# Performance work log

Measured on AMD Instinct MI355X. Metric: run time of the kernel, lower is better.

The kernel has to match this reference:

```python
import jax, jax.numpy as jnp
import numpy as np

NUM_HEADS = 16


def setup_inputs() -> dict:
    key = jax.random.key(0)
    k = jax.random.split(key, 5)
    b, s, h = 2, 2048, 1024
    scale = 1.0 / np.sqrt(h)
    return {
        "x": jax.random.normal(k[0], (b, s, h), dtype=jnp.float32),
        "W_qkv": jax.random.normal(k[1], (h, 3 * h), dtype=jnp.float32) * scale,
        "b_qkv": jax.random.normal(k[2], (3 * h,), dtype=jnp.float32) * 0.02,
        "W_o": jax.random.normal(k[3], (h, h), dtype=jnp.float32) * scale,
        "b_o": jax.random.normal(k[4], (h,), dtype=jnp.float32) * 0.02,
    }


def _mha_causal(Q, K, V, num_heads):
    b, s, hd = Q.shape
    d_head = hd // num_heads
    # b s (n h) -> b n s h
    _Q = Q.reshape(b, s, num_heads, d_head).transpose(0, 2, 1, 3)
    _K = K.reshape(b, s, num_heads, d_head).transpose(0, 2, 1, 3)
    _V = V.reshape(b, s, num_heads, d_head).transpose(0, 2, 1, 3)
    scores = jnp.einsum('bnqh,bnkh->bnqk', _Q, _K)
    causal = jnp.tril(jnp.ones((s, s), dtype=bool))  # True where allowed
    scores = jnp.where(causal, scores, -jnp.inf) / jnp.sqrt(jnp.float32(d_head))
    A = jax.nn.softmax(scores, axis=-1)
    AV = jnp.einsum('bnqk,bnkh->bnqh', A, _V)
    return AV.transpose(0, 2, 1, 3).reshape(b, s, hd)


def reference(x, W_qkv, b_qkv, W_o, b_o):
    qkv = x @ W_qkv + b_qkv  # [b, s, 3h]
    Q, K, V = jnp.split(qkv, 3, axis=-1)
    attn = _mha_causal(Q, K, V, NUM_HEADS)
    return attn @ W_o + b_o
```

## Files before the change

### kernel.cpp

```cpp
#include <hip/hip_runtime.h>
#include <hip/hip_bf16.h>

typedef unsigned short u16;
typedef __attribute__((ext_vector_type(8))) short short8;
typedef __attribute__((ext_vector_type(4))) float f32x4;
typedef __attribute__((ext_vector_type(16))) float f32x16;
typedef __attribute__((ext_vector_type(4))) float float4v;
typedef __attribute__((ext_vector_type(4))) unsigned int uint4v;
typedef __attribute__((ext_vector_type(2))) unsigned int uint2v;

__device__ __forceinline__ u16 f2bf(float f) {
    union { float f; unsigned u; } x;
    x.f = f;
    unsigned r = x.u + 0x7fffu + ((x.u >> 16) & 1u);
    return (u16)(r >> 16);
}

__device__ __forceinline__ unsigned cvtpk(float lo, float hi) {
    unsigned r;
    asm("v_cvt_pk_bf16_f32 %0, %1, %2" : "=v"(r) : "v"(lo), "v"(hi));
    return r;
}

__device__ __forceinline__ void gload16(const u16* g, u16* l) {
    __builtin_amdgcn_global_load_lds(
        (const __attribute__((address_space(1))) unsigned*)g,
        (__attribute__((address_space(3))) unsigned*)l, 16, 0, 0);
}

#define WAITV(n) asm volatile("s_waitcnt vmcnt(" #n ")" ::: "memory")

__global__ __launch_bounds__(256) void prep(
    const float* __restrict__ x, const float* __restrict__ Wqkv,
    const float* __restrict__ Wo, u16* __restrict__ x_bf,
    u16* __restrict__ wqkvT, u16* __restrict__ woT) {
    int bid = blockIdx.x;
    int t = threadIdx.x;
    if (bid < 2048) {
        int i = bid * 256 + t;
        const float4v* s = (const float4v*)(x + (size_t)i * 8);
        float4v a = s[0], b = s[1];
        uint4v o;
        o[0] = (unsigned)f2bf(a[0]) | ((unsigned)f2bf(a[1]) << 16);
        o[1] = (unsigned)f2bf(a[2]) | ((unsigned)f2bf(a[3]) << 16);
        o[2] = (unsigned)f2bf(b[0]) | ((unsigned)f2bf(b[1]) << 16);
        o[3] = (unsigned)f2bf(b[2]) | ((unsigned)f2bf(b[3]) << 16);
        *(uint4v*)(x_bf + (size_t)i * 8) = o;
        return;
    }
    const float* src;
    u16* dst;
    int C, tid;
    if (bid < 2816) { tid = bid - 2048; src = Wqkv; dst = wqkvT; C = 3072; }
    else            { tid = bid - 2816; src = Wo;   dst = woT;   C = 1024; }
    int tr = (tid & 15) * 64;
    int tc = (tid >> 4) * 64;
    __shared__ __align__(16) u16 tile[64][72];
    int r = t >> 2;
    int c4 = (t & 3) * 16;
    const float4v* sp = (const float4v*)(src + (size_t)(tr + r) * C + tc + c4);
#pragma unroll
    for (int v = 0; v < 4; v++) {
        float4v xv = sp[v];
#pragma unroll
        for (int j = 0; j < 4; j++) tile[r][c4 + v * 4 + j] = f2bf(xv[j]);
    }
    __syncthreads();
    u16* dp = dst + (size_t)(tc + r) * 1024 + tr + c4;
#pragma unroll
    for (int i = 0; i < 16; i++) dp[i] = tile[c4 + i][r];
}

__global__ __launch_bounds__(256) void gemm_qkv(
    const u16* __restrict__ A, const u16* __restrict__ BT,
    const float* __restrict__ bias, u16* __restrict__ qbuf,
    u16* __restrict__ kvp) {
    const int K = 1024;
    __shared__ __align__(16) u16 SMEM[24576];
    int bm = blockIdx.x, bn = blockIdx.y;
    int t = threadIdx.x;
    int lane = t & 63, wave = t >> 6;
    int wr = wave >> 1, wc = wave & 1;
    f32x4 acc[4][4] = {};

    const u16* gA = A + (size_t)(bm * 128) * K;
    const u16* gB = BT + (size_t)(bn * 128) * K;

    auto stage = [&](int buf, int k0) {
#pragma unroll
        for (int i = 0; i < 2; i++) {
            int o = i * 4096 + t * 16;
            int row = o >> 6;
            int cb = (o & 63) ^ (((row >> 1) & 3) << 4);
            gload16(gA + (size_t)row * K + k0 + (cb >> 1),
                    &SMEM[buf * 4096 + i * 2048 + (t & 192) * 8]);
        }
#pragma unroll
        for (int i = 0; i < 2; i++) {
            int o = i * 4096 + t * 16;
            int row = o >> 6;
            int cb = (o & 63) ^ (((row >> 1) & 3) << 4);
            gload16(gB + (size_t)row * K + k0 + (cb >> 1),
                    &SMEM[12288 + buf * 4096 + i * 2048 + (t & 192) * 8]);
        }
    };

    stage(0, 0);
    stage(1, 32);
    WAITV(4);
    __builtin_amdgcn_s_barrier();

    for (int tt = 0; tt < 32; tt++) {
        bool pre = (tt + 2 < 32);
        if (pre) stage((tt + 2) % 3, (tt + 2) << 5);
        int row16 = lane & 15;
        int colb = ((lane >> 4) * 16) ^ (((row16 >> 1) & 3) << 4);
        const u16* Ab = &SMEM[(tt % 3) * 4096];
        const u16* Bb = &SMEM[12288 + (tt % 3) * 4096];
        short8 af[4], bf[4];
#pragma unroll
        for (int m = 0; m < 4; m++)
            af[m] = *(const short8*)&Ab[(wr * 64 + m * 16 + row16) * 32 + (colb >> 1)];
#pragma unroll
        for (int n = 0; n < 4; n++)
            bf[n] = *(const short8*)&Bb[(wc * 64 + n * 16 + row16) * 32 + (colb >> 1)];
        __builtin_amdgcn_s_setprio(1);
#pragma unroll
        for (int m = 0; m < 4; m++)
#pragma unroll
            for (int n = 0; n < 4; n++)
                acc[m][n] = __builtin_amdgcn_mfma_f32_16x16x32_bf16(
                    af[m], bf[n], acc[m][n], 0, 0, 0);
        __builtin_amdgcn_s_setprio(0);
        if (pre) { WAITV(4); } else { WAITV(0); }
        __builtin_amdgcn_s_barrier();
    }

    int l15 = lane & 15, hi = lane >> 4;
    if (bn < 8) {
#pragma unroll
        for (int m = 0; m < 4; m++)
#pragma unroll
            for (int n = 0; n < 4; n++) {
                int col = bn * 128 + wc * 64 + n * 16 + l15;
                float bv = bias[col];
#pragma unroll
                for (int r = 0; r < 4; r++) {
                    int row = bm * 128 + wr * 64 + m * 16 + hi * 4 + r;
                    qbuf[(size_t)row * 1024 + col] = f2bf(acc[m][n][r] + bv);
                }
            }
    } else if (bn < 16) {
        int h2 = (bn - 8) * 2 + wc;
#pragma unroll
        for (int m = 0; m < 4; m++)
#pragma unroll
            for (int n = 0; n < 4; n++) {
                int d = n * 16 + l15;
                float bv = bias[1024 + h2 * 64 + d];
#pragma unroll
                for (int r = 0; r < 4; r++) {
                    int row = bm * 128 + wr * 64 + m * 16 + hi * 4 + r;
                    int b = row >> 11;
                    int tt = (row & 2047) >> 6;
                    int k = row & 63;
                    kvp[(size_t)(b * 16 + h2) * 262144 + tt * 8192 + k * 64 + d] =
                        f2bf(acc[m][n][r] + bv);
                }
            }
    } else {
        int h2 = (bn - 16) * 2 + wc;
        int rowbase = bm * 128 + wr * 64;
        int b = rowbase >> 11;
        int tt = (rowbase & 2047) >> 6;
        u16* wl = &SMEM[wave * 4608];
#pragma unroll
        for (int m = 0; m < 4; m++)
#pragma unroll
            for (int n = 0; n < 4; n++) {
                int d = n * 16 + l15;
                float bv = bias[2048 + h2 * 64 + d];
                unsigned p0 = cvtpk(acc[m][n][0] + bv, acc[m][n][1] + bv);
                unsigned p1 = cvtpk(acc[m][n][2] + bv, acc[m][n][3] + bv);
                *(uint2v*)&wl[d * 72 + m * 16 + hi * 4] = (uint2v){p0, p1};
            }
        u16* dst = kvp + (size_t)(b * 16 + h2) * 262144 + tt * 8192 + 4096;
#pragma unroll
        for (int i = 0; i < 8; i++)
            *(uint4v*)(dst + lane * 64 + i * 8) = *(const uint4v*)&wl[lane * 72 + i * 8];
    }
}

__global__ __launch_bounds__(256) void gemm_out(
    const u16* __restrict__ A, const u16* __restrict__ BT,
    const float* __restrict__ bias, float* __restrict__ Cout) {
    const int K = 1024, N = 1024;
    __shared__ __align__(16) u16 As[3][4096];
    __shared__ __align__(16) u16 Bs[3][2048];
    int bm = blockIdx.x, bn = blockIdx.y;
    int t = threadIdx.x;
    int lane = t & 63, wave = t >> 6;
    int wr = wave >> 1, wc = wave & 1;
    f32x4 acc[4][2] = {};

    const u16* gA = A + (size_t)(bm * 128) * K;
    const u16* gB = BT + (size_t)(bn * 64) * K;

    auto stage = [&](int buf, int k0) {
#pragma unroll
        for (int i = 0; i < 2; i++) {
            int o = i * 4096 + t * 16;
            int row = o >> 6;
            int cb = (o & 63) ^ (((row >> 1) & 3) << 4);
            gload16(gA + (size_t)row * K + k0 + (cb >> 1),
                    &As[buf][i * 2048 + (t & 192) * 8]);
        }
        {
            int o = t * 16;
            int row = o >> 6;
            int cb = (o & 63) ^ (((row >> 1) & 3) << 4);
            gload16(gB + (size_t)row * K + k0 + (cb >> 1),
                    &Bs[buf][(t & 192) * 8]);
        }
    };

    stage(0, 0);
    stage(1, 32);
    WAITV(3);
    __builtin_amdgcn_s_barrier();

    for (int tt = 0; tt < 32; tt++) {
        bool pre = (tt + 2 < 32);
        if (pre) stage((tt + 2) % 3, (tt + 2) << 5);
        int row16 = lane & 15;
        int colb = ((lane >> 4) * 16) ^ (((row16 >> 1) & 3) << 4);
        short8 af[4], bf[2];
#pragma unroll
        for (int m = 0; m < 4; m++)
            af[m] = *(const short8*)&As[tt % 3][(wr * 64 + m * 16 + row16) * 32 + (colb >> 1)];
#pragma unroll
        for (int n = 0; n < 2; n++)
            bf[n] = *(const short8*)&Bs[tt % 3][(wc * 32 + n * 16 + row16) * 32 + (colb >> 1)];
        __builtin_amdgcn_s_setprio(1);
#pragma unroll
        for (int m = 0; m < 4; m++)
#pragma unroll
            for (int n = 0; n < 2; n++)
                acc[m][n] = __builtin_amdgcn_mfma_f32_16x16x32_bf16(
                    bf[n], af[m], acc[m][n], 0, 0, 0);
        __builtin_amdgcn_s_setprio(0);
        if (pre) { WAITV(3); } else { WAITV(0); }
        __builtin_amdgcn_s_barrier();
    }

    int l15 = lane & 15, hi = lane >> 4;
#pragma unroll
    for (int m = 0; m < 4; m++)
#pragma unroll
        for (int n = 0; n < 2; n++) {
            int col0 = bn * 64 + wc * 32 + n * 16 + hi * 4;
            float4v bv = *(const float4v*)&bias[col0];
            int row = bm * 128 + wr * 64 + m * 16 + l15;
            float4v v = {acc[m][n][0] + bv[0], acc[m][n][1] + bv[1],
                         acc[m][n][2] + bv[2], acc[m][n][3] + bv[3]};
            *(float4v*)(Cout + (size_t)row * N + col0) = v;
        }
}

__global__ __launch_bounds__(256, 2) void attn_kernel(
    const u16* __restrict__ qbuf, const u16* __restrict__ kvp,
    u16* __restrict__ attn, float* __restrict__ part_o,
    float* __restrict__ part_l) {
    int bid = blockIdx.x;
    int bh = bid & 31;
    int j = 23 - (bid >> 5);
    int sp, tbeg, tend, kc = 0;
    bool partial;
    if (j >= 8) {
        int idx = j - 8;
        sp = 8 + (idx >> 1);
        kc = idx & 1;
        int half = sp + 1;
        partial = true;
        tbeg = kc ? half : 0;
        tend = kc ? 2 * sp + 2 : half;
    } else {
        sp = j;
        partial = false;
        tbeg = 0;
        tend = 2 * sp + 2;
    }
    int b = bh >> 4, h = bh & 15;
    int t = threadIdx.x;
    int lane = t & 63, w = t >> 6;
    int qb = sp * 128 + w * 32;
    int kend = qb + 32;
    int l31 = lane & 31, hi32 = lane >> 5;
    int swz = (lane & 7) << 4;

    __shared__ __align__(16) u16 KVb[24576];

    const u16* kvb = kvp + (size_t)bh * 262144;

    auto stage = [&](int buf, int tt) {
        const char* g0 = (const char*)(kvb + (size_t)tt * 8192);
#pragma unroll
        for (int kv2 = 0; kv2 < 2; kv2++)
#pragma unroll
            for (int i = 0; i < 2; i++) {
                int o = i * 4096 + t * 16;
                int row = o >> 7;
                int cb = (o & 127) ^ ((row & 7) << 4);
                gload16((const u16*)(g0 + kv2 * 8192 + row * 128 + cb),
                        &KVb[buf * 8192 + kv2 * 4096 + i * 2048 + (t & 192) * 8]);
            }
    };

    short8 qf[4];
    {
        const u16* q0 = qbuf + (size_t)(b * 2048 + qb + l31) * 1024 + h * 64 + hi32 * 8;
#pragma unroll
        for (int dd = 0; dd < 4; dd++) qf[dd] = *(const short8*)(q0 + dd * 16);
    }
    stage(tbeg % 3, tbeg);
    stage((tbeg + 1) % 3, tbeg + 1);

    float l_lane = 0.f;
    f32x16 oT[2] = {};

    const float C1 = 0.1803368880f;
    const float C2 = -17.3123404907f;

    WAITV(4);
    __builtin_amdgcn_s_barrier();

    for (int tt = tbeg; tt < tend; tt++) {
        bool pre = (tt + 2 < tend);
        if (pre) stage((tt + 2) % 3, tt + 2);
        int k0 = tt * 64;
        if (k0 < kend) {
            const u16* Ks = &KVb[(tt % 3) * 8192];
            const u16* Vs = Ks + 4096;
            f32x16 sc[2];
            __builtin_amdgcn_s_setprio(1);
#pragma unroll
            for (int kb = 0; kb < 2; kb++) {
                f32x16 z = {};
#pragma unroll
                for (int dd = 0; dd < 4; dd++) {
                    int off = (kb * 32 + l31) * 64 + (((dd * 32 + hi32 * 16) ^ swz) >> 1);
                    short8 kf = *(const short8*)&Ks[off];
                    z = __builtin_amdgcn_mfma_f32_32x32x16_bf16(kf, qf[dd], z, 0, 0, 0);
                }
                sc[kb] = z;
            }
            __builtin_amdgcn_s_setprio(0);

            float p[2][16];
            int q_g = qb + l31;
            if (k0 + 64 > qb) {
#pragma unroll
                for (int kb = 0; kb < 2; kb++)
#pragma unroll
                    for (int r = 0; r < 16; r++) {
                        int kg = k0 + kb * 32 + (r & 3) + 8 * (r >> 2) + 4 * hi32;
                        float v = (kg <= q_g) ? sc[kb][r] : -1e30f;
                        float pe = __builtin_amdgcn_exp2f(fmaf(v, C1, C2));
                        p[kb][r] = pe;
                        l_lane += pe;
                    }
            } else {
#pragma unroll
                for (int kb = 0; kb < 2; kb++)
#pragma unroll
                    for (int r = 0; r < 16; r++) {
                        float pe = __builtin_amdgcn_exp2f(fmaf(sc[kb][r], C1, C2));
                        p[kb][r] = pe;
                        l_lane += pe;
                    }
            }

            short8 pb[4];
#pragma unroll
            for (int kb = 0; kb < 2; kb++)
#pragma unroll
                for (int cset = 0; cset < 2; cset++) {
                    const float* pp = &p[kb][cset * 8];
                    unsigned A0 = cvtpk(pp[0], pp[1]);
                    unsigned A1 = cvtpk(pp[2], pp[3]);
                    unsigned A2 = cvtpk(pp[4], pp[5]);
                    unsigned A3 = cvtpk(pp[6], pp[7]);
                    unsigned za = hi32 ? A0 : A2;
                    unsigned zb = hi32 ? A1 : A3;
                    unsigned sa = (unsigned)__shfl_xor((int)za, 32, 64);
                    unsigned sb = (unsigned)__shfl_xor((int)zb, 32, 64);
                    uint4v wv;
                    wv[0] = hi32 ? sa : A0;
                    wv[1] = hi32 ? sb : A1;
                    wv[2] = hi32 ? A2 : sa;
                    wv[3] = hi32 ? A3 : sb;
                    pb[kb * 2 + cset] = __builtin_bit_cast(short8, wv);
                }

            __builtin_amdgcn_s_setprio(1);
#pragma unroll
            for (int mb = 0; mb < 2; mb++)
#pragma unroll
                for (int kk = 0; kk < 4; kk++) {
                    int off = (mb * 32 + l31) * 64 + (((kk * 32 + hi32 * 16) ^ swz) >> 1);
                    short8 vf = *(const short8*)&Vs[off];
                    oT[mb] = __builtin_amdgcn_mfma_f32_32x32x16_bf16(vf, pb[kk], oT[mb], 0, 0, 0);
                }
            __builtin_amdgcn_s_setprio(0);
        }
        if (pre) { WAITV(4); } else { WAITV(0); }
        __builtin_amdgcn_s_barrier();
    }

    if (partial) {
        int blk = (bh * 8 + (sp - 8)) * 2 + kc;
        float* po = part_o + (size_t)blk * 8192;
        int lr = w * 32 + l31;
        float lf = l_lane + __shfl_xor(l_lane, 32, 64);
        if (hi32 == 0) part_l[blk * 128 + lr] = lf;
#pragma unroll
        for (int mb = 0; mb < 2; mb++)
#pragma unroll
            for (int r = 0; r < 16; r++) {
                int d = mb * 32 + (r & 3) + 8 * (r >> 2) + 4 * hi32;
                po[lr * 64 + d] = oT[mb][r];
            }
        return;
    }

    float lf = l_lane + __shfl_xor(l_lane, 32, 64);
    float linv = __builtin_amdgcn_rcpf(lf);
    u16* gp = attn + (size_t)(b * 2048 + qb + l31) * 1024 + h * 64;
#pragma unroll
    for (int mb = 0; mb < 2; mb++)
#pragma unroll
        for (int g = 0; g < 4; g++) {
            unsigned w0 = cvtpk(oT[mb][4 * g] * linv, oT[mb][4 * g + 1] * linv);
            unsigned w1 = cvtpk(oT[mb][4 * g + 2] * linv, oT[mb][4 * g + 3] * linv);
            int d0 = mb * 32 + g * 8 + hi32 * 4;
            *(uint2v*)(gp + d0) = (uint2v){w0, w1};
        }
}

__global__ __launch_bounds__(256) void attn_merge(
    const float* __restrict__ part_o, const float* __restrict__ part_l,
    u16* __restrict__ attn) {
    int bid = blockIdx.x;
    int bh = bid & 31;
    int sp8 = bid >> 5;
    int sp = sp8 + 8;
    int b = bh >> 4, h = bh & 15;
    int t = threadIdx.x;
    int blk0 = (bh * 8 + sp8) * 2;
    const float* o0 = part_o + (size_t)blk0 * 8192;
    const float* o1 = o0 + 8192;
    const float* l0 = part_l + blk0 * 128;
    const float* l1 = l0 + 128;
#pragma unroll
    for (int i = 0; i < 4; i++) {
        int r = (t >> 3) + i * 32;
        int d0 = (t & 7) * 8;
        float linv = __builtin_amdgcn_rcpf(l0[r] + l1[r]);
        const float* a = o0 + r * 64 + d0;
        const float* c = o1 + r * 64 + d0;
        uint4v w;
#pragma unroll
        for (int k = 0; k < 4; k++)
            w[k] = cvtpk((a[2 * k] + c[2 * k]) * linv,
                         (a[2 * k + 1] + c[2 * k + 1]) * linv);
        u16* gp = attn + (size_t)(b * 2048 + sp * 128 + r) * 1024 + h * 64 + d0;
        *(uint4v*)gp = w;
    }
}

extern "C" void kernel_launch(void* const* d_in, const int* in_sizes, int n_in,
                              void* d_out, int out_size, void* d_ws, size_t ws_size,
                              hipStream_t stream) {
    const float* x    = (const float*)d_in[0];
    const float* Wqkv = (const float*)d_in[1];
    const float* bqkv = (const float*)d_in[2];
    const float* Wo   = (const float*)d_in[3];
    const float* bo   = (const float*)d_in[4];
    float* out = (float*)d_out;

    char* ws = (char*)d_ws;
    u16* x_bf   = (u16*)(ws);
    u16* attnb  = (u16*)(ws);
    u16* wqkvT  = (u16*)(ws + (8ull << 20));
    u16* woT    = (u16*)(ws + (14ull << 20));
    u16* qbuf   = (u16*)(ws + (16ull << 20));
    u16* kvp    = (u16*)(ws + (24ull << 20));
    float* part_o = (float*)(ws + (40ull << 20));
    float* part_l = (float*)(ws + (56ull << 20));

    prep<<<3072, 256, 0, stream>>>(x, Wqkv, Wo, x_bf, wqkvT, woT);
    gemm_qkv<<<dim3(32, 24), 256, 0, stream>>>(x_bf, wqkvT, bqkv, qbuf, kvp);
    attn_kernel<<<768, 256, 0, stream>>>(qbuf, kvp, attnb, part_o, part_l);
    attn_merge<<<256, 256, 0, stream>>>(part_o, part_l, attnb);
    gemm_out<<<dim3(32, 16), 256, 0, stream>>>(attnb, woT, bo, out);
}
```

Baseline: 110.5 us.

## Replace triple-buffered swizzled QKV GEMM staging with single-buffer synchronous loads

```diff
diff --git a/kernel.cpp b/kernel.cpp
--- a/kernel.cpp
+++ b/kernel.cpp
@@ -76,54 +76,38 @@
     const float* __restrict__ bias, u16* __restrict__ qbuf,
     u16* __restrict__ kvp) {
     const int K = 1024;
-    __shared__ __align__(16) u16 SMEM[24576];
+    __shared__ __align__(16) u16 SMEM[18432];
+    u16* As = SMEM;
+    u16* Bs = SMEM + 4096;
     int bm = blockIdx.x, bn = blockIdx.y;
     int t = threadIdx.x;
     int lane = t & 63, wave = t >> 6;
     int wr = wave >> 1, wc = wave & 1;
     f32x4 acc[4][4] = {};
 
+    int lrow = lane >> 2;
+    int lk = (lane & 3) * 8;
     const u16* gA = A + (size_t)(bm * 128) * K;
     const u16* gB = BT + (size_t)(bn * 128) * K;
 
-    auto stage = [&](int buf, int k0) {
+    for (int k0 = 0; k0 < K; k0 += 32) {
+        __syncthreads();
 #pragma unroll
         for (int i = 0; i < 2; i++) {
-            int o = i * 4096 + t * 16;
-            int row = o >> 6;
-            int cb = (o & 63) ^ (((row >> 1) & 3) << 4);
-            gload16(gA + (size_t)row * K + k0 + (cb >> 1),
-                    &SMEM[buf * 4096 + i * 2048 + (t & 192) * 8]);
-        }
-#pragma unroll
-        for (int i = 0; i < 2; i++) {
-            int o = i * 4096 + t * 16;
-            int row = o >> 6;
-            int cb = (o & 63) ^ (((row >> 1) & 3) << 4);
-            gload16(gB + (size_t)row * K + k0 + (cb >> 1),
-                    &SMEM[12288 + buf * 4096 + i * 2048 + (t & 192) * 8]);
-        }
-    };
-
-    stage(0, 0);
-    stage(1, 32);
-    WAITV(4);
-    __builtin_amdgcn_s_barrier();
-
-    for (int tt = 0; tt < 32; tt++) {
-        bool pre = (tt + 2 < 32);
-        if (pre) stage((tt + 2) % 3, (tt + 2) << 5);
-        int row16 = lane & 15;
-        int colb = ((lane >> 4) * 16) ^ (((row16 >> 1) & 3) << 4);
-        const u16* Ab = &SMEM[(tt % 3) * 4096];
-        const u16* Bb = &SMEM[12288 + (tt % 3) * 4096];
+            int ch = wave * 2 + i;
+            int row = ch * 16 + lrow;
+            gload16(gA + (size_t)row * K + k0 + lk, &As[ch * 512]);
+            gload16(gB + (size_t)row * K + k0 + lk, &Bs[ch * 512]);
+        }
+        __syncthreads();
+        int row16 = lane & 15, kg = (lane >> 4) * 8;
         short8 af[4], bf[4];
 #pragma unroll
         for (int m = 0; m < 4; m++)
-            af[m] = *(const short8*)&Ab[(wr * 64 + m * 16 + row16) * 32 + (colb >> 1)];
+            af[m] = *(const short8*)&As[(wr * 64 + m * 16 + row16) * 32 + kg];
 #pragma unroll
         for (int n = 0; n < 4; n++)
-            bf[n] = *(const short8*)&Bb[(wc * 64 + n * 16 + row16) * 32 + (colb >> 1)];
+            bf[n] = *(const short8*)&Bs[(wc * 64 + n * 16 + row16) * 32 + kg];
         __builtin_amdgcn_s_setprio(1);
 #pragma unroll
         for (int m = 0; m < 4; m++)
@@ -132,9 +116,8 @@
                 acc[m][n] = __builtin_amdgcn_mfma_f32_16x16x32_bf16(
                     af[m], bf[n], acc[m][n], 0, 0, 0);
         __builtin_amdgcn_s_setprio(0);
-        if (pre) { WAITV(4); } else { WAITV(0); }
-        __builtin_amdgcn_s_barrier();
-    }
+    }
+    __syncthreads();
 
     int l15 = lane & 15, hi = lane >> 4;
     if (bn < 8) {
```

After: 123.0 us. 1.11x slower.
